# Optimization experiments

Hardware: AMD Instinct MI355X
Metric: run time of the kernel (lower is better)

## Reference

```python
import jax, jax.numpy as jnp
import numpy as np

NORM_EPS = 1e-6


def setup_inputs() -> dict:
    key = jax.random.key(0)
    k1, k2 = jax.random.split(key)
    in_features, out_features = 4096, 4096
    x = jax.random.normal(k1, (2, 2048, in_features), dtype=jnp.float32)
    scale = 1.0 / np.sqrt(in_features)
    weight = jax.random.normal(k2, (out_features, in_features), dtype=jnp.float32) * scale
    norm_weight = jnp.ones((in_features,), dtype=jnp.float32)
    return {"x": x, "weight": weight, "norm_weight": norm_weight}


def reference(x, weight, norm_weight):
    # RMSNorm over the last dim
    rms = jnp.sqrt(jnp.mean(x * x, axis=-1, keepdims=True) + NORM_EPS)
    x_n = x / rms * norm_weight
    # ternary weight quantization (absmean scale alpha)
    alpha = jnp.maximum(jnp.mean(jnp.abs(weight)), 1e-10)
    w_q = jnp.clip(jnp.round(weight / alpha), -1.0, 1.0)
    # per-token int8 activation quantization (absmax scale gamma)
    gamma = jnp.maximum(jnp.max(jnp.abs(x_n), axis=-1, keepdims=True), 1e-10)
    x_q = jnp.clip(jnp.round(x_n * 127.0 / gamma), -128.0, 127.0)
    # rescaled matmul: y = x_q @ w_q.T * (alpha * gamma / 127)
    y = jnp.einsum('bsk,nk->bsn', x_q, w_q) * (alpha * gamma / 127.0)
    return y
```

## Files before the change

### kernel.cpp

```cpp
#include <hip/hip_runtime.h>
#include <cstdint>
#include <cstddef>


#define KD 4096
#define MD 4096
#define ND 4096

#define WBLK 512

typedef int i32x4 __attribute__((ext_vector_type(4)));

__device__ __forceinline__ void gl2lds16(const signed char* g, signed char* l) {
  __builtin_amdgcn_global_load_lds(
      (const __attribute__((address_space(1))) void*)g,
      (__attribute__((address_space(3))) void*)l, 16, 0, 0);
}

__device__ __forceinline__ float wave_sum(float v) {
#pragma unroll
  for (int off = 32; off; off >>= 1) v += __shfl_down(v, off, 64);
  return v;
}
__device__ __forceinline__ float wave_max(float v) {
#pragma unroll
  for (int off = 32; off; off >>= 1) v = fmaxf(v, __shfl_down(v, off, 64));
  return v;
}


__global__ __launch_bounds__(256) void k_alpha_part(const float* __restrict__ w,
                                                    float* __restrict__ part) {
  __shared__ float red[4];
  const int tid = threadIdx.x;
  const float4* w4 = (const float4*)(w + (size_t)blockIdx.x * 4096);
  float s = 0.f;
#pragma unroll
  for (int i = 0; i < 4; ++i) {
    float4 v = w4[i * 256 + tid];
    s += fabsf(v.x) + fabsf(v.y) + fabsf(v.z) + fabsf(v.w);
  }
  s = wave_sum(s);
  if ((tid & 63) == 0) red[tid >> 6] = s;
  __syncthreads();
  if (tid == 0) part[blockIdx.x] = (red[0] + red[1]) + (red[2] + red[3]);
}


__device__ __forceinline__ uint32_t qw4(float4 v, float alpha) {
  int q0 = (int)fminf(fmaxf(rintf(v.x / alpha), -1.f), 1.f);
  int q1 = (int)fminf(fmaxf(rintf(v.y / alpha), -1.f), 1.f);
  int q2 = (int)fminf(fmaxf(rintf(v.z / alpha), -1.f), 1.f);
  int q3 = (int)fminf(fmaxf(rintf(v.w / alpha), -1.f), 1.f);
  return (uint32_t)(q0 & 255) | ((uint32_t)(q1 & 255) << 8) |
         ((uint32_t)(q2 & 255) << 16) | ((uint32_t)(q3 & 255) << 24);
}

__global__ __launch_bounds__(256) void k_quant_all(const float* __restrict__ w,
                                                   const float* __restrict__ x,
                                                   const float* __restrict__ nw,
                                                   const float* __restrict__ part,
                                                   signed char* __restrict__ wq,
                                                   signed char* __restrict__ xq,
                                                   float* __restrict__ gamma,
                                                   float* __restrict__ alpha_out) {
  const int tid = threadIdx.x;
  const int bid = blockIdx.x;
  __shared__ float red[4];
  __shared__ float red2[4];

  if (bid < 4096) {
    const int row = bid;
    const float4* x4 = (const float4*)(x + (size_t)row * 4096);
    const float4* n4 = (const float4*)nw;
    float4 xv[4], nv[4];
#pragma unroll
    for (int i = 0; i < 4; ++i) {
      xv[i] = x4[i * 256 + tid];
      nv[i] = n4[i * 256 + tid];
    }
    float ss = 0.f, mx = 0.f;
#pragma unroll
    for (int i = 0; i < 4; ++i) {
      ss += xv[i].x * xv[i].x + xv[i].y * xv[i].y + xv[i].z * xv[i].z +
            xv[i].w * xv[i].w;
      mx = fmaxf(mx,
                 fmaxf(fmaxf(fabsf(xv[i].x * nv[i].x), fabsf(xv[i].y * nv[i].y)),
                       fmaxf(fabsf(xv[i].z * nv[i].z), fabsf(xv[i].w * nv[i].w))));
    }
    ss = wave_sum(ss);
    mx = wave_max(mx);
    if ((tid & 63) == 0) {
      red[tid >> 6] = ss;
      red2[tid >> 6] = mx;
    }
    __syncthreads();
    const float tot = (red[0] + red[1]) + (red[2] + red[3]);
    const float rms = sqrtf(tot * (1.0f / 4096.0f) + 1e-6f);
    const float mxr = fmaxf(fmaxf(red2[0], red2[1]), fmaxf(red2[2], red2[3]));
    const float g = fmaxf(mxr / rms, 1e-10f);
    if (tid == 0) gamma[row] = g;
    const float inv = 127.0f / (rms * g);

    uint32_t* xqi = (uint32_t*)(xq + (size_t)row * 4096);
#pragma unroll
    for (int i = 0; i < 4; ++i) {
      const int f = i * 256 + tid;
      int q0 = (int)fminf(fmaxf(rintf(xv[i].x * nv[i].x * inv), -128.f), 127.f);
      int q1 = (int)fminf(fmaxf(rintf(xv[i].y * nv[i].y * inv), -128.f), 127.f);
      int q2 = (int)fminf(fmaxf(rintf(xv[i].z * nv[i].z * inv), -128.f), 127.f);
      int q3 = (int)fminf(fmaxf(rintf(xv[i].w * nv[i].w * inv), -128.f), 127.f);
      xqi[f] = (uint32_t)(q0 & 255) | ((uint32_t)(q1 & 255) << 8) |
               ((uint32_t)(q2 & 255) << 16) | ((uint32_t)(q3 & 255) << 24);
    }
  } else {
    const int wb = bid - 4096;
    float s = 0.f;
#pragma unroll
    for (int i = 0; i < 16; ++i) s += part[i * 256 + tid];
    s = wave_sum(s);
    if ((tid & 63) == 0) red[tid >> 6] = s;
    __syncthreads();
    const float alpha =
        fmaxf(((red[0] + red[1]) + (red[2] + red[3])) * (1.0f / 16777216.0f),
              1e-10f);
    if (wb == 0 && tid == 0) alpha_out[0] = alpha;

    const float4* w4 = (const float4*)w;
    uint32_t* wqi = (uint32_t*)wq;
#pragma unroll 1
    for (int k = 0; k < 32; k += 4) {
      const int f0 = (wb * 32 + k) * 256 + tid;
      float4 v0 = w4[f0];
      float4 v1 = w4[f0 + 256];
      float4 v2 = w4[f0 + 512];
      float4 v3 = w4[f0 + 768];
      wqi[f0] = qw4(v0, alpha);
      wqi[f0 + 256] = qw4(v1, alpha);
      wqi[f0 + 512] = qw4(v2, alpha);
      wqi[f0 + 768] = qw4(v3, alpha);
    }
  }
}


__global__ __launch_bounds__(256) void k_gemm(const signed char* __restrict__ xq,
                                              const signed char* __restrict__ wq,
                                              const float* __restrict__ gamma,
                                              const float* __restrict__ alpha_p,
                                              float* __restrict__ out) {
  __shared__ __align__(16) signed char As[128 * 128];
  __shared__ __align__(16) signed char Bs[128 * 128];
  const int tid = threadIdx.x;
  const int lane = tid & 63;
  const int wave = tid >> 6;
  const int wm = (wave >> 1) * 64;
  const int wn = (wave & 1) * 64;
  const int quad = lane >> 4;
  const int l16 = lane & 15;
  const int bm = blockIdx.y * 128;
  const int bn = blockIdx.x * 128;

  const signed char* Ag = xq + (size_t)bm * KD;
  const signed char* Bg = wq + (size_t)bn * KD;

  const int lr = lane >> 3;
  const int sc = (lane & 7) ^ lr;
  const signed char* agp[4];
  const signed char* bgp[4];
  signed char* la[4];
  signed char* lb[4];
#pragma unroll
  for (int i = 0; i < 4; ++i) {
    const int R = i * 32 + wave * 8 + lr;
    agp[i] = Ag + (size_t)R * KD + sc * 16;
    bgp[i] = Bg + (size_t)R * KD + sc * 16;
    la[i] = &As[(i * 32 + wave * 8) * 128];
    lb[i] = &Bs[(i * 32 + wave * 8) * 128];
  }

  i32x4 acc[4][4];
#pragma unroll
  for (int i = 0; i < 4; ++i)
#pragma unroll
    for (int j = 0; j < 4; ++j) acc[i][j] = (i32x4){0, 0, 0, 0};

  const int swz = l16 & 7;

  for (int k0 = 0; k0 < KD; k0 += 128) {
    __syncthreads();
#pragma unroll
    for (int i = 0; i < 4; ++i) gl2lds16(agp[i] + k0, la[i]);
#pragma unroll
    for (int i = 0; i < 4; ++i) gl2lds16(bgp[i] + k0, lb[i]);
    __syncthreads();

#pragma unroll
    for (int ks = 0; ks < 2; ++ks) {
      const int pos = ((ks * 4 + quad) ^ swz) * 16;
      i32x4 af[4], bf[4];
#pragma unroll
      for (int mi = 0; mi < 4; ++mi)
        af[mi] = *(const i32x4*)&As[(wm + mi * 16 + l16) * 128 + pos];
#pragma unroll
      for (int ni = 0; ni < 4; ++ni)
        bf[ni] = *(const i32x4*)&Bs[(wn + ni * 16 + l16) * 128 + pos];
#pragma unroll
      for (int mi = 0; mi < 4; ++mi)
#pragma unroll
        for (int ni = 0; ni < 4; ++ni)
          acc[mi][ni] = __builtin_amdgcn_mfma_i32_16x16x64_i8(af[mi], bf[ni],
                                                              acc[mi][ni], 0, 0, 0);
    }
  }

  const float alpha = alpha_p[0];
#pragma unroll
  for (int mi = 0; mi < 4; ++mi) {
#pragma unroll
    for (int r = 0; r < 4; ++r) {
      const int m = bm + wm + mi * 16 + quad * 4 + r;
      const float s = (alpha * gamma[m]) / 127.0f;
#pragma unroll
      for (int ni = 0; ni < 4; ++ni) {
        const int n = bn + wn + ni * 16 + l16;
        out[(size_t)m * ND + n] = (float)acc[mi][ni][r] * s;
      }
    }
  }
}


extern "C" void kernel_launch(void* const* d_in, const int* in_sizes, int n_in,
                              void* d_out, int out_size, void* d_ws, size_t ws_size,
                              hipStream_t stream) {
  const float* x = (const float*)d_in[0];
  const float* w = (const float*)d_in[1];
  const float* nw = (const float*)d_in[2];
  float* out = (float*)d_out;

  char* ws = (char*)d_ws;
  signed char* xq = (signed char*)ws;
  signed char* wq = (signed char*)(ws + ((size_t)1 << 24));
  float* gamma = (float*)(ws + ((size_t)2 << 24));
  float* part = (float*)(ws + ((size_t)2 << 24) + 16384);
  float* alpha = (float*)(ws + ((size_t)2 << 24) + 32768);

  k_alpha_part<<<4096, 256, 0, stream>>>(w, part);
  k_quant_all<<<4096 + WBLK, 256, 0, stream>>>(w, x, nw, part, wq, xq, gamma, alpha);
  dim3 g(ND / 128, MD / 128);
  k_gemm<<<g, 256, 0, stream>>>(xq, wq, gamma, alpha, out);
}
```

Baseline: 240.4 us.

## Rewrite int8 GEMM with 256x256 tiles, double-buffered LDS and interleaved prefetch

```diff
diff --git a/kernel.cpp b/kernel.cpp
--- a/kernel.cpp
+++ b/kernel.cpp
@@ -144,79 +144,101 @@
 }
 
 
-__global__ __launch_bounds__(256) void k_gemm(const signed char* __restrict__ xq,
-                                              const signed char* __restrict__ wq,
-                                              const float* __restrict__ gamma,
-                                              const float* __restrict__ alpha_p,
-                                              float* __restrict__ out) {
-  __shared__ __align__(16) signed char As[128 * 128];
-  __shared__ __align__(16) signed char Bs[128 * 128];
+#define BM 256
+#define BN 256
+#define BK 64
+
+__global__ __launch_bounds__(512, 2) void k_gemm(const signed char* __restrict__ xq,
+                                                 const signed char* __restrict__ wq,
+                                                 const float* __restrict__ gamma,
+                                                 const float* __restrict__ alpha_p,
+                                                 float* __restrict__ out) {
+  __shared__ __align__(16) signed char LDS_[65536];
   const int tid = threadIdx.x;
   const int lane = tid & 63;
   const int wave = tid >> 6;
-  const int wm = (wave >> 1) * 64;
-  const int wn = (wave & 1) * 64;
+  const int wm = (wave >> 2) * 128;
+  const int wn = (wave & 3) * 64;
   const int quad = lane >> 4;
   const int l16 = lane & 15;
-  const int bm = blockIdx.y * 128;
-  const int bn = blockIdx.x * 128;
-
-  const signed char* Ag = xq + (size_t)bm * KD;
-  const signed char* Bg = wq + (size_t)bn * KD;
-
-  const int lr = lane >> 3;
-  const int sc = (lane & 7) ^ lr;
-  const signed char* agp[4];
-  const signed char* bgp[4];
-  signed char* la[4];
-  signed char* lb[4];
-#pragma unroll
-  for (int i = 0; i < 4; ++i) {
-    const int R = i * 32 + wave * 8 + lr;
-    agp[i] = Ag + (size_t)R * KD + sc * 16;
-    bgp[i] = Bg + (size_t)R * KD + sc * 16;
-    la[i] = &As[(i * 32 + wave * 8) * 128];
-    lb[i] = &Bs[(i * 32 + wave * 8) * 128];
-  }
-
-  i32x4 acc[4][4];
-#pragma unroll
-  for (int i = 0; i < 4; ++i)
+
+  const int bid = (blockIdx.x & 7) * 32 + (blockIdx.x >> 3);
+  const int bm = (bid >> 4) * BM;
+  const int bn = (bid & 15) * BN;
+
+  const int lr = lane >> 2;
+  const int sc = (lane & 3) ^ ((lane >> 3) & 3);
+  const int rb0 = wave * 16;
+  const int rb1 = (8 + wave) * 16;
+  const signed char* ag0 = xq + (size_t)(bm + rb0 + lr) * KD + sc * 16;
+  const signed char* ag1 = xq + (size_t)(bm + rb1 + lr) * KD + sc * 16;
+  const signed char* bg0 = wq + (size_t)(bn + rb0 + lr) * KD + sc * 16;
+  const signed char* bg1 = wq + (size_t)(bn + rb1 + lr) * KD + sc * 16;
+  const int lA0 = rb0 * BK;
+  const int lA1 = rb1 * BK;
+
+  const int pos = (quad ^ ((l16 >> 1) & 3)) * 16;
+
+  i32x4 acc[8][4];
+#pragma unroll
+  for (int i = 0; i < 8; ++i)
 #pragma unroll
     for (int j = 0; j < 4; ++j) acc[i][j] = (i32x4){0, 0, 0, 0};
 
-  const int swz = l16 & 7;
-
-  for (int k0 = 0; k0 < KD; k0 += 128) {
+  gl2lds16(ag0, LDS_ + lA0);
+  gl2lds16(ag1, LDS_ + lA1);
+  gl2lds16(bg0, LDS_ + 16384 + lA0);
+  gl2lds16(bg1, LDS_ + 16384 + lA1);
+  __syncthreads();
+
+  for (int t = 0; t < 64; ++t) {
+    const int c = t & 1;
+    const signed char* Ab = LDS_ + c * 32768;
+    const signed char* Bb = Ab + 16384;
+    signed char* An = LDS_ + (c ^ 1) * 32768;
+    signed char* Bn = An + 16384;
+    const size_t kn = (size_t)(t + 1) * BK;
+    const bool more = (t < 63);
+
+    i32x4 bf[4], af[2];
+
+#pragma unroll
+    for (int p = 0; p < 4; ++p) {
+      if (p == 0) {
+#pragma unroll
+        for (int ni = 0; ni < 4; ++ni)
+          bf[ni] = *(const i32x4*)&Bb[(wn + ni * 16 + l16) * BK + pos];
+      }
+#pragma unroll
+      for (int j = 0; j < 2; ++j)
+        af[j] = *(const i32x4*)&Ab[(wm + (p * 2 + j) * 16 + l16) * BK + pos];
+
+      if (more) {
+        if (p == 0) {
+          gl2lds16(ag0 + kn, An + lA0);
+          gl2lds16(ag1 + kn, An + lA1);
+        } else if (p == 1) {
+          gl2lds16(bg0 + kn, Bn + lA0);
+          gl2lds16(bg1 + kn, Bn + lA1);
+        }
+      }
+      __builtin_amdgcn_s_barrier();
+      __builtin_amdgcn_s_setprio(1);
+#pragma unroll
+      for (int j = 0; j < 2; ++j)
+#pragma unroll
+        for (int ni = 0; ni < 4; ++ni)
+          acc[p * 2 + j][ni] = __builtin_amdgcn_mfma_i32_16x16x64_i8(
+              af[j], bf[ni], acc[p * 2 + j][ni], 0, 0, 0);
+      __builtin_amdgcn_s_setprio(0);
+      if (p < 3) __builtin_amdgcn_s_barrier();
+    }
     __syncthreads();
-#pragma unroll
-    for (int i = 0; i < 4; ++i) gl2lds16(agp[i] + k0, la[i]);
-#pragma unroll
-    for (int i = 0; i < 4; ++i) gl2lds16(bgp[i] + k0, lb[i]);
-    __syncthreads();
-
-#pragma unroll
-    for (int ks = 0; ks < 2; ++ks) {
-      const int pos = ((ks * 4 + quad) ^ swz) * 16;
-      i32x4 af[4], bf[4];
-#pragma unroll
-      for (int mi = 0; mi < 4; ++mi)
-        af[mi] = *(const i32x4*)&As[(wm + mi * 16 + l16) * 128 + pos];
-#pragma unroll
-      for (int ni = 0; ni < 4; ++ni)
-        bf[ni] = *(const i32x4*)&Bs[(wn + ni * 16 + l16) * 128 + pos];
-#pragma unroll
-      for (int mi = 0; mi < 4; ++mi)
-#pragma unroll
-        for (int ni = 0; ni < 4; ++ni)
-          acc[mi][ni] = __builtin_amdgcn_mfma_i32_16x16x64_i8(af[mi], bf[ni],
-                                                              acc[mi][ni], 0, 0, 0);
-    }
   }
 
   const float alpha = alpha_p[0];
 #pragma unroll
-  for (int mi = 0; mi < 4; ++mi) {
+  for (int mi = 0; mi < 8; ++mi) {
 #pragma unroll
     for (int r = 0; r < 4; ++r) {
       const int m = bm + wm + mi * 16 + quad * 4 + r;
@@ -248,6 +270,5 @@
 
   k_alpha_part<<<4096, 256, 0, stream>>>(w, part);
   k_quant_all<<<4096 + WBLK, 256, 0, stream>>>(w, x, nw, part, wq, xq, gamma, alpha);
-  dim3 g(ND / 128, MD / 128);
-  k_gemm<<<g, 256, 0, stream>>>(xq, wq, gamma, alpha, out);
-}
+  k_gemm<<<dim3(256), dim3(512), 0, stream>>>(xq, wq, gamma, alpha, out);
+}
```

Result: no change. 235.9 us (-1.9%).
